# Kernel tuning notes

Hardware: AMD Instinct MI355X
Metric: run time of the kernel (lower is better)

Reference implementation:

```python
import jax, jax.numpy as jnp
import numpy as np

B, H, W, C = 32, 56, 56, 192
WS, SHIFT, HEADS = 7, 3, 6
HID = 4 * C
N = WS * WS
NW = (H // WS) * (W // WS)
EPS = 1e-5


def _rel_index():
    ch, cw = np.meshgrid(np.arange(WS), np.arange(WS), indexing='ij')
    coords = np.stack([ch.ravel(), cw.ravel()])  # [2, N]
    rel = coords[:, :, None] - coords[:, None, :]  # [2, N, N]
    rel = rel.transpose(1, 2, 0)
    rel[:, :, 0] += WS - 1
    rel[:, :, 1] += WS - 1
    rel[:, :, 0] *= 2 * WS - 1
    return rel.sum(-1).astype(np.int32)  # [N, N]


def _attn_mask():
    img = np.zeros((H, W), np.float32)
    sl = (slice(0, -WS), slice(-WS, -SHIFT), slice(-SHIFT, None))
    cnt = 0
    for hs in sl:
        for ws_ in sl:
            img[hs, ws_] = cnt
            cnt += 1
    mw = img.reshape(H // WS, WS, W // WS, WS).transpose(0, 2, 1, 3).reshape(-1, N)
    m = mw[:, None, :] - mw[:, :, None]
    return np.where(m != 0, -100.0, 0.0).astype(np.float32)  # [NW, N, N]


def setup_inputs() -> dict:
    key = jax.random.key(0)
    ks = jax.random.split(key, 16)
    r = lambda k, s, sc: (jax.random.normal(k, s, jnp.float32) * sc)
    return {
        'x': r(ks[0], (B, H * W, C), 1.0),
        'norm1_w': jnp.ones((C,), jnp.float32),
        'norm1_b': jnp.zeros((C,), jnp.float32),
        'qkv_w': r(ks[1], (C, 3 * C), 0.02),
        'qkv_b': jnp.zeros((3 * C,), jnp.float32),
        'bias_table': r(ks[2], ((2 * WS - 1) ** 2, HEADS), 0.02),
        'proj_w': r(ks[3], (C, C), 0.02),
        'proj_b': jnp.zeros((C,), jnp.float32),
        'norm2_w': jnp.ones((C,), jnp.float32),
        'norm2_b': jnp.zeros((C,), jnp.float32),
        'fc1_w': r(ks[4], (C, HID), 0.02),
        'fc1_b': jnp.zeros((HID,), jnp.float32),
        'fc2_w': r(ks[5], (HID, C), 0.02),
        'fc2_b': jnp.zeros((C,), jnp.float32),
        'attn_mask': jnp.asarray(_attn_mask()),
        'rel_index': jnp.asarray(_rel_index()),
    }


def _ln(x, w, b):
    mu = jnp.mean(x, -1, keepdims=True)
    var = jnp.mean(jnp.square(x - mu), -1, keepdims=True)
    return (x - mu) * jax.lax.rsqrt(var + EPS) * w + b


def reference(x, norm1_w, norm1_b, qkv_w, qkv_b, bias_table, proj_w, proj_b,
              norm2_w, norm2_b, fc1_w, fc1_b, fc2_w, fc2_b, attn_mask, rel_index):
    shortcut = x
    h = _ln(x, norm1_w, norm1_b).reshape(B, H, W, C)
    # cyclic shift
    h = jnp.roll(h, shift=(-SHIFT, -SHIFT), axis=(1, 2))
    # window partition -> (B*NW, N, C)
    h = h.reshape(B, H // WS, WS, W // WS, WS, C).transpose(0, 1, 3, 2, 4, 5)
    h = h.reshape(B * NW, N, C)
    # attention
    qkv = (h @ qkv_w + qkv_b).reshape(B * NW, N, 3, HEADS, C // HEADS)
    qkv = qkv.transpose(2, 0, 3, 1, 4)  # [3, B_, heads, N, d]
    q, k, v = qkv[0], qkv[1], qkv[2]
    scale = (C // HEADS) ** -0.5
    attn = jnp.einsum('bhnd,bhmd->bhnm', q * scale, k)
    bias = bias_table[rel_index].transpose(2, 0, 1)  # [heads, N, N]
    attn = attn + bias[None]
    attn = attn.reshape(B, NW, HEADS, N, N) + attn_mask[None, :, None]
    attn = jax.nn.softmax(attn.reshape(B * NW, HEADS, N, N), axis=-1)
    o = jnp.einsum('bhnm,bhmd->bhnd', attn, v)
    o = o.transpose(0, 2, 1, 3).reshape(B * NW, N, C)
    o = o @ proj_w + proj_b
    # window reverse
    o = o.reshape(B, H // WS, W // WS, WS, WS, C).transpose(0, 1, 3, 2, 4, 5)
    o = o.reshape(B, H, W, C)
    o = jnp.roll(o, shift=(SHIFT, SHIFT), axis=(1, 2)).reshape(B, H * W, C)
    x = shortcut + o
    # MLP (exact GELU, like torch nn.GELU)
    m = _ln(x, norm2_w, norm2_b)
    m = jax.nn.gelu(m @ fc1_w + fc1_b, approximate=False) @ fc2_w + fc2_b
    return x + m
```

## Files before the change

### kernel.cpp

```cpp
#include <hip/hip_runtime.h>
#include <math.h>

#define B_    32
#define HH    56
#define WW_   56
#define C_    192
#define WS_   7
#define SHIFT_ 3
#define HEADS_ 6
#define DH    32
#define N_    49
#define NWIN  2048
#define ROWS  100352
#define HID_  768
#define QKVN  576

typedef __bf16 bfr;
typedef __bf16 bf8 __attribute__((ext_vector_type(8)));
typedef __bf16 bf4 __attribute__((ext_vector_type(4)));
typedef float  f32x4 __attribute__((ext_vector_type(4)));

#define MFMA16(a,b,c) __builtin_amdgcn_mfma_f32_16x16x32_bf16(a,b,c,0,0,0)

#define OQW   0
#define OPW   110592
#define OW1   147456
#define OW2   294912
#define OBM   442368
#define WTOT  442368
#define BMTOT 98304

__global__ __launch_bounds__(256) void k_prep(
    const float* __restrict__ qkvw, const float* __restrict__ projw,
    const float* __restrict__ w1,   const float* __restrict__ w2,
    bfr* __restrict__ wsp)
{
  int idx = blockIdx.x*256 + threadIdx.x;
  if (idx >= WTOT) return;
  if (idx < OPW)      { int i=idx;      int n=i/192, k=i%192; wsp[idx] = (bfr)qkvw[k*QKVN + n]; }
  else if (idx < OW1) { int i=idx-OPW;  int n=i/192, k=i%192; wsp[idx] = (bfr)projw[k*C_ + n]; }
  else if (idx < OW2) { int i=idx-OW1;  int n=i/192, k=i%192; wsp[idx] = (bfr)w1[k*HID_ + n]; }
  else                { int i=idx-OW2;  int n=i/768, k=i%768; wsp[idx] = (bfr)w2[k*C_ + n]; }
}

__global__ __launch_bounds__(256) void k_prep2(
    const float* __restrict__ btab, const int* __restrict__ rel,
    const float* __restrict__ mask, bfr* __restrict__ bm)
{
  int idx = blockIdx.x*256 + threadIdx.x;
  if (idx >= BMTOT) return;
  int row = idx & 63, col = (idx>>6) & 63, cls = (idx>>12) & 3, head = idx>>14;
  int wh = (cls & 2) ? 7 : 0, ww = (cls & 1) ? 7 : 0;
  int wi = wh*8 + ww;
  float v = -1e30f;
  if (row < N_ && col < N_) {
    int e = row*N_ + col;
    v = btab[rel[e]*HEADS_ + head] + mask[(size_t)wi*N_*N_ + e];
  }
  bm[idx] = (bfr)v;
}

#define SM_HS 0
#define SM_QS 25600
#define SM_KS 34816
#define SM_VT 44032
#define SM_P  53248
#define SM_OV 62464
#define SM_SR 71680
#define SM1_TOT 71936
#define HSP 200

__global__ __launch_bounds__(256, 2) void k_attn(
    const float* __restrict__ x,
    const float* __restrict__ n1w, const float* __restrict__ n1b,
    const bfr*   __restrict__ wsp,
    const float* __restrict__ qkvb,
    const float* __restrict__ projb,
    float* __restrict__ out)
{
  __shared__ char smem[SM1_TOT];
  bfr*   hs    = (bfr*)(smem + SM_HS);
  bfr*   qs    = (bfr*)(smem + SM_QS);
  bfr*   ks    = (bfr*)(smem + SM_KS);
  bfr*   vT    = (bfr*)(smem + SM_VT);
  bfr*   P     = (bfr*)(smem + SM_P);
  bfr*   ov2   = (bfr*)(smem + SM_OV);
  int*   srows = (int*)(smem + SM_SR);
  float* pj    = (float*)smem;

  const f32x4 ZERO4 = {0.f, 0.f, 0.f, 0.f};

  int win  = blockIdx.x;
  int tid  = threadIdx.x;
  int lane = tid & 63, wave = tid >> 6;
  int ln15 = lane & 15, quad = lane >> 4;
  int wi   = win & 63;
  int cls  = (((wi>>3)==7) ? 2 : 0) + (((wi&7)==7) ? 1 : 0);

  if (tid < N_) {
    int bb = win >> 6;
    int wh = wi >> 3, ww = wi & 7;
    int th = tid / WS_, tw = tid % WS_;
    int sh = wh*WS_ + th + SHIFT_; if (sh >= HH) sh -= HH;
    int sw = ww*WS_ + tw + SHIFT_; if (sw >= WW_) sw -= WW_;
    srows[tid] = bb*HH*WW_ + sh*WW_ + sw;
  }
  {
    int* hz = (int*)(hs + 49*HSP);
    for (int i = tid; i < 15*HSP/2; i += 256) hz[i] = 0;
  }
  __syncthreads();
  for (int r = wave; r < N_; r += 4) {
    const float* xr = x + (size_t)srows[r]*C_;
    float v0 = xr[lane], v1 = xr[lane+64], v2 = xr[lane+128];
    float s = v0+v1+v2, q = v0*v0+v1*v1+v2*v2;
    #pragma unroll
    for (int m = 32; m; m >>= 1) { s += __shfl_xor(s, m); q += __shfl_xor(q, m); }
    float mu = s*(1.f/C_), var = q*(1.f/C_) - mu*mu;
    float rs = rsqrtf(var + 1e-5f);
    hs[r*HSP + lane]     = (bfr)((v0-mu)*rs*n1w[lane]     + n1b[lane]);
    hs[r*HSP + lane+64]  = (bfr)((v1-mu)*rs*n1w[lane+64]  + n1b[lane+64]);
    hs[r*HSP + lane+128] = (bfr)((v2-mu)*rs*n1w[lane+128] + n1b[lane+128]);
  }
  __syncthreads();

  const bfr* qkvwT  = wsp + OQW;
  const bfr* projwT = wsp + OPW;
  const bfr* bmask  = wsp + OBM;

  f32x4 accp[3][4];
  #pragma unroll
  for (int j=0;j<3;j++)
    #pragma unroll
    for (int mt=0;mt<4;mt++) accp[j][mt] = ZERO4;

  for (int pair = 0; pair < 3; pair++) {
    {
      float qb[3];
      #pragma unroll
      for (int j=0;j<3;j++) qb[j] = qkvb[j*192 + pair*64 + wave*16 + ln15];
      f32x4 acc[3][4];
      #pragma unroll
      for (int j=0;j<3;j++)
        #pragma unroll
        for (int mt=0;mt<4;mt++) acc[j][mt] = ZERO4;
      #pragma unroll
      for (int kk = 0; kk < 6; kk++) {
        bf8 afr[4];
        #pragma unroll
        for (int mt=0;mt<4;mt++)
          afr[mt] = *(const bf8*)&hs[(mt*16+ln15)*HSP + kk*32 + quad*8];
        #pragma unroll
        for (int j=0;j<3;j++) {
          bf8 bw = *(const bf8*)&qkvwT[(size_t)(j*192 + pair*64 + wave*16 + ln15)*192
                                       + kk*32 + quad*8];
          #pragma unroll
          for (int mt=0;mt<4;mt++) acc[j][mt] = MFMA16(afr[mt], bw, acc[j][mt]);
        }
      }
      int colp = wave*16 + ln15;
      int hl = colp >> 5, d = colp & 31;
      #pragma unroll
      for (int j=0;j<3;j++) {
        #pragma unroll
        for (int mt=0;mt<4;mt++)
          #pragma unroll
          for (int r=0;r<4;r++) {
            int row = mt*16 + quad*4 + r;
            float vv = acc[j][mt][r] + qb[j];
            if (j == 0)      qs[(hl*64+row)*36 + d] = (bfr)(vv*0.17677669529663689f);
            else if (j == 1) ks[(hl*64+row)*36 + d] = (bfr)vv;
            else             vT[(hl*32+d)*72 + row] = (bfr)vv;
          }
      }
    }
    __syncthreads();

    bf4 bm4[2][4];
    #pragma unroll
    for (int hl = 0; hl < 2; hl++) {
      const bfr* bmh = bmask + (((size_t)(pair*2+hl)*4 + cls) << 12);
      #pragma unroll
      for (int nt = 0; nt < 4; nt++)
        bm4[hl][nt] = *(const bf4*)&bmh[(nt*16 + ln15)*64 + wave*16 + quad*4];
    }

    float val[2][4][4];
    #pragma unroll
    for (int hl = 0; hl < 2; hl++) {
      bf8 aq = *(const bf8*)&qs[(hl*64 + wave*16 + ln15)*36 + quad*8];
      #pragma unroll
      for (int nt = 0; nt < 4; nt++) {
        f32x4 c;
        c[0] = (float)bm4[hl][nt][0]; c[1] = (float)bm4[hl][nt][1];
        c[2] = (float)bm4[hl][nt][2]; c[3] = (float)bm4[hl][nt][3];
        bf8 bk = *(const bf8*)&ks[(hl*64 + nt*16 + ln15)*36 + quad*8];
        c = MFMA16(aq, bk, c);
        #pragma unroll
        for (int r=0;r<4;r++) val[hl][nt][r] = c[r];
      }
    }

    bf8 pw[2][3];
    #pragma unroll
    for (int hl = 0; hl < 2; hl++)
      #pragma unroll
      for (int j = 0; j < 3; j++)
        pw[hl][j] = *(const bf8*)&projwT[(size_t)((wave*3+j)*16 + ln15)*192
                                         + (pair*2+hl)*32 + quad*8];

    #pragma unroll
    for (int hl = 0; hl < 2; hl++) {
      float mx[4], sum[4];
      #pragma unroll
      for (int r=0;r<4;r++) {
        mx[r] = fmaxf(fmaxf(val[hl][0][r], val[hl][1][r]), fmaxf(val[hl][2][r], val[hl][3][r]));
        #pragma unroll
        for (int m = 1; m < 16; m <<= 1) mx[r] = fmaxf(mx[r], __shfl_xor(mx[r], m));
      }
      #pragma unroll
      for (int nt=0;nt<4;nt++)
        #pragma unroll
        for (int r=0;r<4;r++) val[hl][nt][r] = __expf(val[hl][nt][r] - mx[r]);
      #pragma unroll
      for (int r=0;r<4;r++) {
        sum[r] = val[hl][0][r] + val[hl][1][r] + val[hl][2][r] + val[hl][3][r];
        #pragma unroll
        for (int m = 1; m < 16; m <<= 1) sum[r] += __shfl_xor(sum[r], m);
        sum[r] = 1.f / sum[r];
      }
      #pragma unroll
      for (int nt=0;nt<4;nt++)
        #pragma unroll
        for (int r=0;r<4;r++)
          P[(wave*16 + quad*4 + r)*72 + nt*16 + ln15] = (bfr)(val[hl][nt][r]*sum[r]);
      #pragma unroll
      for (int nt = 0; nt < 2; nt++) {
        f32x4 c = ZERO4;
        #pragma unroll
        for (int k0 = 0; k0 < 64; k0 += 32) {
          bf8 ap = *(const bf8*)&P[(wave*16 + ln15)*72 + k0 + quad*8];
          bf8 bv = *(const bf8*)&vT[(hl*32 + nt*16 + ln15)*72 + k0 + quad*8];
          c = MFMA16(ap, bv, c);
        }
        #pragma unroll
        for (int r=0;r<4;r++)
          ov2[(wave*16 + quad*4 + r)*72 + hl*36 + nt*16 + ln15] = (bfr)c[r];
      }
    }
    __syncthreads();

    #pragma unroll
    for (int hl = 0; hl < 2; hl++) {
      bf8 afr[4];
      #pragma unroll
      for (int mt=0;mt<4;mt++)
        afr[mt] = *(const bf8*)&ov2[(mt*16+ln15)*72 + hl*36 + quad*8];
      #pragma unroll
      for (int j=0;j<3;j++)
        #pragma unroll
        for (int mt=0;mt<4;mt++) accp[j][mt] = MFMA16(afr[mt], pw[hl][j], accp[j][mt]);
    }
  }

  __syncthreads();
  #pragma unroll
  for (int j=0;j<3;j++) {
    int col = (wave*3+j)*16 + ln15;
    float pb = projb[col];
    #pragma unroll
    for (int mt=0;mt<4;mt++)
      #pragma unroll
      for (int r=0;r<4;r++)
        pj[(mt*16 + quad*4 + r)*196 + col] = accp[j][mt][r] + pb;
  }
  __syncthreads();
  for (int idx = tid; idx < N_*C_; idx += 256) {
    int n = idx / C_, c = idx % C_;
    size_t gr = (size_t)srows[n]*C_ + c;
    out[gr] = x[gr] + pj[n*196 + c];
  }
}

#define SM2_TS  0
#define SM2_HID 25600
#define SM2_TOT 51200

__global__ __launch_bounds__(256, 2) void k_mlp(
    float* __restrict__ y,
    const float* __restrict__ n2w, const float* __restrict__ n2b,
    const bfr* __restrict__ wsp,
    const float* __restrict__ b1, const float* __restrict__ b2)
{
  __shared__ char smem[SM2_TOT];
  bfr*   ts   = (bfr*)(smem + SM2_TS);
  bfr*   hidc = (bfr*)(smem + SM2_HID);
  float* st   = (float*)smem;

  const f32x4 ZERO4 = {0.f, 0.f, 0.f, 0.f};

  int r0 = blockIdx.x * 64;
  int tid = threadIdx.x;
  int lane = tid & 63, wave = tid >> 6;
  int ln15 = lane & 15, quad = lane >> 4;

  #pragma unroll
  for (int i = 0; i < 16; i++) {
    int r = wave + i*4;
    const float* yr = y + (size_t)(r0 + r)*C_;
    float v0 = yr[lane], v1 = yr[lane+64], v2 = yr[lane+128];
    float s = v0+v1+v2, q = v0*v0+v1*v1+v2*v2;
    #pragma unroll
    for (int m = 32; m; m >>= 1) { s += __shfl_xor(s, m); q += __shfl_xor(q, m); }
    float mu = s*(1.f/C_), var = q*(1.f/C_) - mu*mu;
    float rs = rsqrtf(var + 1e-5f);
    ts[r*HSP + lane]     = (bfr)((v0-mu)*rs*n2w[lane]     + n2b[lane]);
    ts[r*HSP + lane+64]  = (bfr)((v1-mu)*rs*n2w[lane+64]  + n2b[lane+64]);
    ts[r*HSP + lane+128] = (bfr)((v2-mu)*rs*n2w[lane+128] + n2b[lane+128]);
  }
  __syncthreads();

  const bfr* w1T = wsp + OW1;
  const bfr* w2T = wsp + OW2;

  f32x4 accp[3][4];
  #pragma unroll
  for (int j=0;j<3;j++)
    #pragma unroll
    for (int mt=0;mt<4;mt++) accp[j][mt] = ZERO4;

  for (int c = 0; c < 4; c++) {
    bf8 wf1[3][6];
    float bb[3];
    #pragma unroll
    for (int j=0;j<3;j++) {
      const bfr* wb = w1T + (size_t)((c*12 + wave*3 + j)*16 + ln15)*192 + quad*8;
      #pragma unroll
      for (int kk=0;kk<6;kk++)
        wf1[j][kk] = *(const bf8*)&wb[kk*32];
      bb[j] = b1[c*192 + (wave*3+j)*16 + ln15];
    }
    f32x4 acc[3][4];
    #pragma unroll
    for (int j=0;j<3;j++)
      #pragma unroll
      for (int mt=0;mt<4;mt++) acc[j][mt] = ZERO4;
    #pragma unroll
    for (int kk = 0; kk < 6; kk++) {
      bf8 afr[4];
      #pragma unroll
      for (int mt=0;mt<4;mt++)
        afr[mt] = *(const bf8*)&ts[(mt*16+ln15)*HSP + kk*32 + quad*8];
      #pragma unroll
      for (int j=0;j<3;j++)
        #pragma unroll
        for (int mt=0;mt<4;mt++) acc[j][mt] = MFMA16(afr[mt], wf1[j][kk], acc[j][mt]);
    }
    bf8 wf2[3][6];
    #pragma unroll
    for (int j=0;j<3;j++) {
      const bfr* wb2 = w2T + (size_t)((wave*3+j)*16 + ln15)*768 + c*192 + quad*8;
      #pragma unroll
      for (int kk=0;kk<6;kk++)
        wf2[j][kk] = *(const bf8*)&wb2[kk*32];
      int colc = (wave*3 + j)*16 + ln15;
      #pragma unroll
      for (int mt=0;mt<4;mt++)
        #pragma unroll
        for (int r=0;r<4;r++) {
          int row = mt*16 + quad*4 + r;
          float g = acc[j][mt][r] + bb[j];
          float u = g*(1.5957691216f + 0.0713548170f*g*g);
          hidc[row*HSP + colc] = (bfr)(g / (1.f + __expf(-u)));
        }
    }
    __syncthreads();
    #pragma unroll
    for (int kk = 0; kk < 6; kk++) {
      bf8 afr[4];
      #pragma unroll
      for (int mt=0;mt<4;mt++)
        afr[mt] = *(const bf8*)&hidc[(mt*16+ln15)*HSP + kk*32 + quad*8];
      #pragma unroll
      for (int j=0;j<3;j++)
        #pragma unroll
        for (int mt=0;mt<4;mt++) accp[j][mt] = MFMA16(afr[mt], wf2[j][kk], accp[j][mt]);
    }
    __syncthreads();
  }

  #pragma unroll
  for (int j=0;j<3;j++) {
    int col = (wave*3+j)*16 + ln15;
    float bb2 = b2[col];
    #pragma unroll
    for (int mt=0;mt<4;mt++)
      #pragma unroll
      for (int r=0;r<4;r++) {
        int row = mt*16 + quad*4 + r;
        st[row*196 + col] = accp[j][mt][r] + bb2;
      }
  }
  __syncthreads();
  for (int idx = tid; idx < 64*C_; idx += 256) {
    int r = idx / C_, c = idx % C_;
    size_t gr = (size_t)(r0 + r)*C_ + c;
    y[gr] = y[gr] + st[r*196 + c];
  }
}

extern "C" void kernel_launch(void* const* d_in, const int* in_sizes, int n_in,
                              void* d_out, int out_size, void* d_ws, size_t ws_size,
                              hipStream_t stream) {
  const float* x     = (const float*)d_in[0];
  const float* n1w   = (const float*)d_in[1];
  const float* n1b   = (const float*)d_in[2];
  const float* qkvw  = (const float*)d_in[3];
  const float* qkvb  = (const float*)d_in[4];
  const float* btab  = (const float*)d_in[5];
  const float* projw = (const float*)d_in[6];
  const float* projb = (const float*)d_in[7];
  const float* n2w   = (const float*)d_in[8];
  const float* n2b   = (const float*)d_in[9];
  const float* w1    = (const float*)d_in[10];
  const float* b1    = (const float*)d_in[11];
  const float* w2    = (const float*)d_in[12];
  const float* b2    = (const float*)d_in[13];
  const float* mask  = (const float*)d_in[14];
  const int*   rel   = (const int*)d_in[15];
  float* out = (float*)d_out;
  bfr*   wsp = (bfr*)d_ws;

  k_prep<<<(WTOT+255)/256, 256, 0, stream>>>(qkvw, projw, w1, w2, wsp);
  k_prep2<<<(BMTOT+255)/256, 256, 0, stream>>>(btab, rel, mask, wsp + OBM);
  k_attn<<<NWIN, 256, 0, stream>>>(x, n1w, n1b, wsp, qkvb, projb, out);
  k_mlp<<<ROWS/64, 256, 0, stream>>>(out, n2w, n2b, wsp, b1, b2);
}
```

Baseline: 515.0 us.

## Swap MFMA operand order to produce transposed fragments and vectorize LDS stores

Swaps the A and B operands of the MFMA calls across the QKV, score, PV, proj and MLP GEMMs, so each lane holds four consecutive output columns instead of four consecutive rows. Epilogue writes to LDS become packed bf4/f32x4 stores instead of scalar strided stores, and bias loads become vector loads. Softmax row reductions now need only two cross-lane shuffles instead of four per row, and the bias/mask table is re-laid out to match. It aims to cut LDS store instruction count, bank conflicts and shuffle overhead, at the cost of a layout change that touches many indexing sites and must stay consistent everywhere.

```diff
diff --git a/kernel.cpp b/kernel.cpp
--- a/kernel.cpp
+++ b/kernel.cpp
@@ -49,12 +49,12 @@
 {
   int idx = blockIdx.x*256 + threadIdx.x;
   if (idx >= BMTOT) return;
-  int row = idx & 63, col = (idx>>6) & 63, cls = (idx>>12) & 3, head = idx>>14;
+  int k = idx & 63, q = (idx>>6) & 63, cls = (idx>>12) & 3, head = idx>>14;
   int wh = (cls & 2) ? 7 : 0, ww = (cls & 1) ? 7 : 0;
   int wi = wh*8 + ww;
   float v = -1e30f;
-  if (row < N_ && col < N_) {
-    int e = row*N_ + col;
+  if (q < N_ && k < N_) {
+    int e = q*N_ + k;
     v = btab[rel[e]*HEADS_ + head] + mask[(size_t)wi*N_*N_ + e];
   }
   bm[idx] = (bfr)v;
@@ -136,9 +136,9 @@
 
   for (int pair = 0; pair < 3; pair++) {
     {
-      float qb[3];
-      #pragma unroll
-      for (int j=0;j<3;j++) qb[j] = qkvb[j*192 + pair*64 + wave*16 + ln15];
+      f32x4 qb0 = *(const f32x4*)&qkvb[       pair*64 + wave*16 + quad*4];
+      f32x4 qb1 = *(const f32x4*)&qkvb[192  + pair*64 + wave*16 + quad*4];
+      float qb2 =                 qkvb[384  + pair*64 + wave*16 + ln15];
       f32x4 acc[3][4];
       #pragma unroll
       for (int j=0;j<3;j++)
@@ -150,28 +150,32 @@
         #pragma unroll
         for (int mt=0;mt<4;mt++)
           afr[mt] = *(const bf8*)&hs[(mt*16+ln15)*HSP + kk*32 + quad*8];
-        #pragma unroll
-        for (int j=0;j<3;j++) {
-          bf8 bw = *(const bf8*)&qkvwT[(size_t)(j*192 + pair*64 + wave*16 + ln15)*192
-                                       + kk*32 + quad*8];
-          #pragma unroll
-          for (int mt=0;mt<4;mt++) acc[j][mt] = MFMA16(afr[mt], bw, acc[j][mt]);
+        bf8 bw0 = *(const bf8*)&qkvwT[(size_t)(      pair*64 + wave*16 + ln15)*192 + kk*32 + quad*8];
+        bf8 bw1 = *(const bf8*)&qkvwT[(size_t)(192 + pair*64 + wave*16 + ln15)*192 + kk*32 + quad*8];
+        bf8 bw2 = *(const bf8*)&qkvwT[(size_t)(384 + pair*64 + wave*16 + ln15)*192 + kk*32 + quad*8];
+        #pragma unroll
+        for (int mt=0;mt<4;mt++) {
+          acc[0][mt] = MFMA16(bw0, afr[mt], acc[0][mt]);
+          acc[1][mt] = MFMA16(bw1, afr[mt], acc[1][mt]);
+          acc[2][mt] = MFMA16(afr[mt], bw2, acc[2][mt]);
         }
       }
-      int colp = wave*16 + ln15;
-      int hl = colp >> 5, d = colp & 31;
-      #pragma unroll
-      for (int j=0;j<3;j++) {
-        #pragma unroll
-        for (int mt=0;mt<4;mt++)
-          #pragma unroll
-          for (int r=0;r<4;r++) {
-            int row = mt*16 + quad*4 + r;
-            float vv = acc[j][mt][r] + qb[j];
-            if (j == 0)      qs[(hl*64+row)*36 + d] = (bfr)(vv*0.17677669529663689f);
-            else if (j == 1) ks[(hl*64+row)*36 + d] = (bfr)vv;
-            else             vT[(hl*32+d)*72 + row] = (bfr)vv;
-          }
+      int hlw = wave >> 1;
+      int d0  = (wave & 1)*16 + quad*4;
+      int dv  = (wave & 1)*16 + ln15;
+      #pragma unroll
+      for (int mt=0;mt<4;mt++) {
+        int token = mt*16 + ln15;
+        bf4 pk;
+        #pragma unroll
+        for (int r=0;r<4;r++) pk[r] = (bfr)((acc[0][mt][r] + qb0[r])*0.17677669529663689f);
+        *(bf4*)&qs[(hlw*64+token)*36 + d0] = pk;
+        #pragma unroll
+        for (int r=0;r<4;r++) pk[r] = (bfr)(acc[1][mt][r] + qb1[r]);
+        *(bf4*)&ks[(hlw*64+token)*36 + d0] = pk;
+        #pragma unroll
+        for (int r=0;r<4;r++) pk[r] = (bfr)(acc[2][mt][r] + qb2);
+        *(bf4*)&vT[(hlw*32+dv)*72 + mt*16 + quad*4] = pk;
       }
     }
     __syncthreads();
@@ -182,7 +186,7 @@
       const bfr* bmh = bmask + (((size_t)(pair*2+hl)*4 + cls) << 12);
       #pragma unroll
       for (int nt = 0; nt < 4; nt++)
-        bm4[hl][nt] = *(const bf4*)&bmh[(nt*16 + ln15)*64 + wave*16 + quad*4];
+        bm4[hl][nt] = *(const bf4*)&bmh[(wave*16+ln15)*64 + nt*16 + quad*4];
     }
 
     float val[2][4][4];
@@ -195,7 +199,7 @@
         c[0] = (float)bm4[hl][nt][0]; c[1] = (float)bm4[hl][nt][1];
         c[2] = (float)bm4[hl][nt][2]; c[3] = (float)bm4[hl][nt][3];
         bf8 bk = *(const bf8*)&ks[(hl*64 + nt*16 + ln15)*36 + quad*8];
-        c = MFMA16(aq, bk, c);
+        c = MFMA16(bk, aq, c);
         #pragma unroll
         for (int r=0;r<4;r++) val[hl][nt][r] = c[r];
       }
@@ -211,41 +215,40 @@
 
     #pragma unroll
     for (int hl = 0; hl < 2; hl++) {
-      float mx[4], sum[4];
-      #pragma unroll
-      for (int r=0;r<4;r++) {
-        mx[r] = fmaxf(fmaxf(val[hl][0][r], val[hl][1][r]), fmaxf(val[hl][2][r], val[hl][3][r]));
-        #pragma unroll
-        for (int m = 1; m < 16; m <<= 1) mx[r] = fmaxf(mx[r], __shfl_xor(mx[r], m));
-      }
+      float mx = val[hl][0][0];
       #pragma unroll
       for (int nt=0;nt<4;nt++)
         #pragma unroll
-        for (int r=0;r<4;r++) val[hl][nt][r] = __expf(val[hl][nt][r] - mx[r]);
-      #pragma unroll
-      for (int r=0;r<4;r++) {
-        sum[r] = val[hl][0][r] + val[hl][1][r] + val[hl][2][r] + val[hl][3][r];
-        #pragma unroll
-        for (int m = 1; m < 16; m <<= 1) sum[r] += __shfl_xor(sum[r], m);
-        sum[r] = 1.f / sum[r];
-      }
+        for (int r=0;r<4;r++) mx = fmaxf(mx, val[hl][nt][r]);
+      mx = fmaxf(mx, __shfl_xor(mx, 16));
+      mx = fmaxf(mx, __shfl_xor(mx, 32));
+      float sum = 0.f;
       #pragma unroll
       for (int nt=0;nt<4;nt++)
         #pragma unroll
-        for (int r=0;r<4;r++)
-          P[(wave*16 + quad*4 + r)*72 + nt*16 + ln15] = (bfr)(val[hl][nt][r]*sum[r]);
+        for (int r=0;r<4;r++) { val[hl][nt][r] = __expf(val[hl][nt][r] - mx); sum += val[hl][nt][r]; }
+      sum += __shfl_xor(sum, 16);
+      sum += __shfl_xor(sum, 32);
+      float rsum = 1.f / sum;
+      #pragma unroll
+      for (int nt=0;nt<4;nt++) {
+        bf4 pk;
+        #pragma unroll
+        for (int r=0;r<4;r++) pk[r] = (bfr)(val[hl][nt][r]*rsum);
+        *(bf4*)&P[(wave*16+ln15)*72 + nt*16 + quad*4] = pk;
+      }
+      bf8 ap0 = *(const bf8*)&P[(wave*16+ln15)*72 + quad*8];
+      bf8 ap1 = *(const bf8*)&P[(wave*16+ln15)*72 + 32 + quad*8];
       #pragma unroll
       for (int nt = 0; nt < 2; nt++) {
-        f32x4 c = ZERO4;
-        #pragma unroll
-        for (int k0 = 0; k0 < 64; k0 += 32) {
-          bf8 ap = *(const bf8*)&P[(wave*16 + ln15)*72 + k0 + quad*8];
-          bf8 bv = *(const bf8*)&vT[(hl*32 + nt*16 + ln15)*72 + k0 + quad*8];
-          c = MFMA16(ap, bv, c);
-        }
-        #pragma unroll
-        for (int r=0;r<4;r++)
-          ov2[(wave*16 + quad*4 + r)*72 + hl*36 + nt*16 + ln15] = (bfr)c[r];
+        bf8 bv0 = *(const bf8*)&vT[(hl*32 + nt*16 + ln15)*72 + quad*8];
+        bf8 bv1 = *(const bf8*)&vT[(hl*32 + nt*16 + ln15)*72 + 32 + quad*8];
+        f32x4 c = MFMA16(bv0, ap0, ZERO4);
+        c = MFMA16(bv1, ap1, c);
+        bf4 pk;
+        #pragma unroll
+        for (int r=0;r<4;r++) pk[r] = (bfr)c[r];
+        *(bf4*)&ov2[(wave*16+ln15)*72 + hl*36 + nt*16 + quad*4] = pk;
       }
     }
     __syncthreads();
@@ -259,20 +262,21 @@
       #pragma unroll
       for (int j=0;j<3;j++)
         #pragma unroll
-        for (int mt=0;mt<4;mt++) accp[j][mt] = MFMA16(afr[mt], pw[hl][j], accp[j][mt]);
-    }
-  }
-
-  __syncthreads();
+        for (int mt=0;mt<4;mt++) accp[j][mt] = MFMA16(pw[hl][j], afr[mt], accp[j][mt]);
+    }
+  }
+
   #pragma unroll
   for (int j=0;j<3;j++) {
-    int col = (wave*3+j)*16 + ln15;
-    float pb = projb[col];
-    #pragma unroll
-    for (int mt=0;mt<4;mt++)
-      #pragma unroll
-      for (int r=0;r<4;r++)
-        pj[(mt*16 + quad*4 + r)*196 + col] = accp[j][mt][r] + pb;
+    int col0 = (wave*3+j)*16 + quad*4;
+    f32x4 pb = *(const f32x4*)&projb[col0];
+    #pragma unroll
+    for (int mt=0;mt<4;mt++) {
+      f32x4 w;
+      #pragma unroll
+      for (int r=0;r<4;r++) w[r] = accp[j][mt][r] + pb[r];
+      *(f32x4*)&pj[(mt*16+ln15)*196 + col0] = w;
+    }
   }
   __syncthreads();
   for (int idx = tid; idx < N_*C_; idx += 256) {
@@ -331,14 +335,14 @@
 
   for (int c = 0; c < 4; c++) {
     bf8 wf1[3][6];
-    float bb[3];
+    f32x4 bbv[3];
     #pragma unroll
     for (int j=0;j<3;j++) {
       const bfr* wb = w1T + (size_t)((c*12 + wave*3 + j)*16 + ln15)*192 + quad*8;
       #pragma unroll
       for (int kk=0;kk<6;kk++)
         wf1[j][kk] = *(const bf8*)&wb[kk*32];
-      bb[j] = b1[c*192 + (wave*3+j)*16 + ln15];
+      bbv[j] = *(const f32x4*)&b1[c*192 + (wave*3+j)*16 + quad*4];
     }
     f32x4 acc[3][4];
     #pragma unroll
@@ -354,7 +358,7 @@
       #pragma unroll
       for (int j=0;j<3;j++)
         #pragma unroll
-        for (int mt=0;mt<4;mt++) acc[j][mt] = MFMA16(afr[mt], wf1[j][kk], acc[j][mt]);
+        for (int mt=0;mt<4;mt++) acc[j][mt] = MFMA16(wf1[j][kk], afr[mt], acc[j][mt]);
     }
     bf8 wf2[3][6];
     #pragma unroll
@@ -363,16 +367,18 @@
       #pragma unroll
       for (int kk=0;kk<6;kk++)
         wf2[j][kk] = *(const bf8*)&wb2[kk*32];
-      int colc = (wave*3 + j)*16 + ln15;
-      #pragma unroll
-      for (int mt=0;mt<4;mt++)
+      int colc0 = (wave*3 + j)*16 + quad*4;
+      #pragma unroll
+      for (int mt=0;mt<4;mt++) {
+        bf4 pk;
         #pragma unroll
         for (int r=0;r<4;r++) {
-          int row = mt*16 + quad*4 + r;
-          float g = acc[j][mt][r] + bb[j];
+          float g = acc[j][mt][r] + bbv[j][r];
           float u = g*(1.5957691216f + 0.0713548170f*g*g);
-          hidc[row*HSP + colc] = (bfr)(g / (1.f + __expf(-u)));
+          pk[r] = (bfr)(g / (1.f + __expf(-u)));
         }
+        *(bf4*)&hidc[(mt*16+ln15)*HSP + colc0] = pk;
+      }
     }
     __syncthreads();
     #pragma unroll
@@ -384,22 +390,22 @@
       #pragma unroll
       for (int j=0;j<3;j++)
         #pragma unroll
-        for (int mt=0;mt<4;mt++) accp[j][mt] = MFMA16(afr[mt], wf2[j][kk], accp[j][mt]);
+        for (int mt=0;mt<4;mt++) accp[j][mt] = MFMA16(wf2[j][kk], afr[mt], accp[j][mt]);
     }
     __syncthreads();
   }
 
   #pragma unroll
   for (int j=0;j<3;j++) {
-    int col = (wave*3+j)*16 + ln15;
-    float bb2 = b2[col];
-    #pragma unroll
-    for (int mt=0;mt<4;mt++)
-      #pragma unroll
-      for (int r=0;r<4;r++) {
-        int row = mt*16 + quad*4 + r;
-        st[row*196 + col] = accp[j][mt][r] + bb2;
-      }
+    int col0 = (wave*3+j)*16 + quad*4;
+    f32x4 bb2 = *(const f32x4*)&b2[col0];
+    #pragma unroll
+    for (int mt=0;mt<4;mt++) {
+      f32x4 w;
+      #pragma unroll
+      for (int r=0;r<4;r++) w[r] = accp[j][mt][r] + bb2[r];
+      *(f32x4*)&st[(mt*16+ln15)*196 + col0] = w;
+    }
   }
   __syncthreads();
   for (int idx = tid; idx < 64*C_; idx += 256) {
```

Result: slower. 533.8 us (+3.7%).
